# Kernel tuning notes

Measured on AMD Instinct MI355X. Metric: run time of the kernel, lower is better.

Reference implementation:

```python
import jax, jax.numpy as jnp
import numpy as np

TIME_STEPS = 100
SPIKE_THRESHOLD = 0.5
INPUT_DIM = 8192


def setup_inputs() -> dict:
    key = jax.random.key(0)
    k_x, k_w = jax.random.split(key)
    x = jax.random.uniform(k_x, (INPUT_DIM,), dtype=jnp.float32)
    # matches nn.Parameter(torch.rand(D, D) * 0.01)
    synaptic_weights = jax.random.uniform(k_w, (INPUT_DIM, INPUT_DIM), dtype=jnp.float32) * 0.01
    # matches nn.Parameter(torch.zeros(D))
    membrane_potential = jnp.zeros((INPUT_DIM,), dtype=jnp.float32)
    return {"x": x, "synaptic_weights": synaptic_weights, "membrane_potential": membrane_potential}


def reference(x, synaptic_weights, membrane_potential):
    # Drive is identical every timestep (x and W are loop-invariant), so compute once.
    drive = x @ synaptic_weights  # [D]

    def step(pot, _):
        pot = pot + drive
        spike = (pot >= SPIKE_THRESHOLD).astype(pot.dtype)  # spike_mask.float()
        pot = pot * (1.0 - spike)  # membrane_potential[spike_mask] = 0
        return pot, (spike, pot)

    _, (spikes, potentials) = jax.lax.scan(step, membrane_potential, None, length=TIME_STEPS)
    synaptic_activity = jnp.abs(synaptic_weights).mean()
    # spikes: [T, D], potentials: [T, D], synaptic_activity: scalar
    return spikes, potentials, synaptic_activity
```

## Files before the change

kernel.cpp:

```cpp
#include <hip/hip_runtime.h>

#define D 8192
#define T_STEPS 100
#define SPIKE_THR 0.5f
#define BLOCK 256
#define COLS_PER_THREAD 4
#define NCHUNK 256
#define ROWS_PER_CHUNK (D / NCHUNK)
#define COLBLOCKS (D / (BLOCK * COLS_PER_THREAD))

__global__ void __launch_bounds__(BLOCK)
k_partial(const float* __restrict__ x, const float* __restrict__ W,
          float* __restrict__ ws_drive, float* __restrict__ ws_abs) {
    __shared__ float xs[ROWS_PER_CHUNK];
    __shared__ float red[BLOCK];

    const int chunk = blockIdx.y;
    const int row0  = chunk * ROWS_PER_CHUNK;
    if (threadIdx.x < ROWS_PER_CHUNK)
        xs[threadIdx.x] = x[row0 + threadIdx.x];
    __syncthreads();

    const int j0 = (blockIdx.x * BLOCK + threadIdx.x) * COLS_PER_THREAD;

    float ax = 0.f, ay = 0.f, az = 0.f, aw = 0.f;
    float asum = 0.f;
    #pragma unroll
    for (int i = 0; i < ROWS_PER_CHUNK; ++i) {
        const float xv = xs[i];
        const float4 w = *reinterpret_cast<const float4*>(
            &W[(size_t)(row0 + i) * D + j0]);
        ax = fmaf(xv, w.x, ax);
        ay = fmaf(xv, w.y, ay);
        az = fmaf(xv, w.z, az);
        aw = fmaf(xv, w.w, aw);
        asum += fabsf(w.x) + fabsf(w.y) + fabsf(w.z) + fabsf(w.w);
    }

    float4 acc; acc.x = ax; acc.y = ay; acc.z = az; acc.w = aw;
    *reinterpret_cast<float4*>(&ws_drive[(size_t)chunk * D + j0]) = acc;

    red[threadIdx.x] = asum;
    __syncthreads();
    for (int s = BLOCK / 2; s > 0; s >>= 1) {
        if (threadIdx.x < s) red[threadIdx.x] += red[threadIdx.x + s];
        __syncthreads();
    }
    if (threadIdx.x == 0)
        ws_abs[blockIdx.y * gridDim.x + blockIdx.x] = red[0];
}

__global__ void __launch_bounds__(BLOCK)
k_sim(const float* __restrict__ ws_drive, const float* __restrict__ ws_abs,
      const float* __restrict__ pot0, float* __restrict__ out) {
    if (blockIdx.x == COLBLOCKS) {
        __shared__ float red[BLOCK];
        const int n = NCHUNK * COLBLOCKS;
        float s = 0.f;
        for (int i = threadIdx.x; i < n; i += BLOCK) s += ws_abs[i];
        red[threadIdx.x] = s;
        __syncthreads();
        for (int st = BLOCK / 2; st > 0; st >>= 1) {
            if (threadIdx.x < st) red[threadIdx.x] += red[threadIdx.x + st];
            __syncthreads();
        }
        if (threadIdx.x == 0)
            out[(size_t)2 * T_STEPS * D] = red[0] / ((float)D * (float)D);
        return;
    }

    const int j0 = (blockIdx.x * BLOCK + threadIdx.x) * COLS_PER_THREAD;

    float dx = 0.f, dy = 0.f, dz = 0.f, dw = 0.f;
    #pragma unroll 8
    for (int c = 0; c < NCHUNK; ++c) {
        const float4 p = *reinterpret_cast<const float4*>(
            &ws_drive[(size_t)c * D + j0]);
        dx += p.x; dy += p.y; dz += p.z; dw += p.w;
    }

    const float4 p0 = *reinterpret_cast<const float4*>(&pot0[j0]);
    float px = p0.x, py = p0.y, pz = p0.z, pw = p0.w;

    float* __restrict__ spikes = out;
    float* __restrict__ pots   = out + (size_t)T_STEPS * D;

    for (int t = 0; t < T_STEPS; ++t) {
        px += dx; py += dy; pz += dz; pw += dw;
        float4 sp;
        sp.x = (px >= SPIKE_THR) ? 1.f : 0.f;
        sp.y = (py >= SPIKE_THR) ? 1.f : 0.f;
        sp.z = (pz >= SPIKE_THR) ? 1.f : 0.f;
        sp.w = (pw >= SPIKE_THR) ? 1.f : 0.f;
        px *= (1.f - sp.x); py *= (1.f - sp.y);
        pz *= (1.f - sp.z); pw *= (1.f - sp.w);
        *reinterpret_cast<float4*>(&spikes[(size_t)t * D + j0]) = sp;
        float4 pv; pv.x = px; pv.y = py; pv.z = pz; pv.w = pw;
        *reinterpret_cast<float4*>(&pots[(size_t)t * D + j0]) = pv;
    }
}

extern "C" void kernel_launch(void* const* d_in, const int* in_sizes, int n_in,
                              void* d_out, int out_size, void* d_ws, size_t ws_size,
                              hipStream_t stream) {
    const float* x   = (const float*)d_in[0];
    const float* W   = (const float*)d_in[1];
    const float* mp0 = (const float*)d_in[2];
    float* out = (float*)d_out;

    float* ws_drive = (float*)d_ws;
    float* ws_abs   = ws_drive + (size_t)NCHUNK * D;

    dim3 g1(COLBLOCKS, NCHUNK);
    k_partial<<<g1, BLOCK, 0, stream>>>(x, W, ws_drive, ws_abs);
    k_sim<<<COLBLOCKS + 1, BLOCK, 0, stream>>>(ws_drive, ws_abs, mp0, out);
}
```

Before: 67.58 us.

## Split drive reduction into own kernel and parallelize simulation over time chunks

Moves the cross-chunk drive reduction into a separate k_reduce kernel (33 blocks) that writes one drive vector. The simulation kernel then runs on a 2D grid over column blocks and chunks of 4 timesteps. Each block replays the earlier timesteps in registers so it can write its own chunk without a serial dependency. The aim is to spread the 6.5 MB of spike and potential output writes across many more blocks than the previous 8, at the cost of an extra launch and redundant recomputation. The unroll count in k_partial also drops from full to 8.

After: 66.25 us. 2.0% less time.

```diff
diff --git a/kernel.cpp b/kernel.cpp
--- a/kernel.cpp
+++ b/kernel.cpp
@@ -8,6 +8,8 @@
 #define NCHUNK 256
 #define ROWS_PER_CHUNK (D / NCHUNK)
 #define COLBLOCKS (D / (BLOCK * COLS_PER_THREAD))
+#define STEPS_PER 4
+#define TCHUNKS (T_STEPS / STEPS_PER)
 
 __global__ void __launch_bounds__(BLOCK)
 k_partial(const float* __restrict__ x, const float* __restrict__ W,
@@ -25,7 +27,7 @@
 
     float ax = 0.f, ay = 0.f, az = 0.f, aw = 0.f;
     float asum = 0.f;
-    #pragma unroll
+    #pragma unroll 8
     for (int i = 0; i < ROWS_PER_CHUNK; ++i) {
         const float xv = xs[i];
         const float4 w = *reinterpret_cast<const float4*>(
@@ -51,9 +53,9 @@
 }
 
 __global__ void __launch_bounds__(BLOCK)
-k_sim(const float* __restrict__ ws_drive, const float* __restrict__ ws_abs,
-      const float* __restrict__ pot0, float* __restrict__ out) {
-    if (blockIdx.x == COLBLOCKS) {
+k_reduce(const float* __restrict__ ws_drive, const float* __restrict__ ws_abs,
+         float* __restrict__ drive, float* __restrict__ out) {
+    if (blockIdx.x == 32) {
         __shared__ float red[BLOCK];
         const int n = NCHUNK * COLBLOCKS;
         float s = 0.f;
@@ -68,25 +70,39 @@
             out[(size_t)2 * T_STEPS * D] = red[0] / ((float)D * (float)D);
         return;
     }
+    const int j = blockIdx.x * BLOCK + threadIdx.x;
+    float s = 0.f;
+    #pragma unroll 8
+    for (int c = 0; c < NCHUNK; ++c)
+        s += ws_drive[(size_t)c * D + j];
+    drive[j] = s;
+}
 
+__global__ void __launch_bounds__(BLOCK)
+k_sim(const float* __restrict__ drive, const float* __restrict__ pot0,
+      float* __restrict__ out) {
     const int j0 = (blockIdx.x * BLOCK + threadIdx.x) * COLS_PER_THREAD;
+    const int t0 = blockIdx.y * STEPS_PER;
 
-    float dx = 0.f, dy = 0.f, dz = 0.f, dw = 0.f;
-    #pragma unroll 8
-    for (int c = 0; c < NCHUNK; ++c) {
-        const float4 p = *reinterpret_cast<const float4*>(
-            &ws_drive[(size_t)c * D + j0]);
-        dx += p.x; dy += p.y; dz += p.z; dw += p.w;
-    }
-
+    const float4 d  = *reinterpret_cast<const float4*>(&drive[j0]);
     const float4 p0 = *reinterpret_cast<const float4*>(&pot0[j0]);
     float px = p0.x, py = p0.y, pz = p0.z, pw = p0.w;
+
+    for (int t = 0; t < t0; ++t) {
+        px += d.x; py += d.y; pz += d.z; pw += d.w;
+        px = (px >= SPIKE_THR) ? 0.f : px;
+        py = (py >= SPIKE_THR) ? 0.f : py;
+        pz = (pz >= SPIKE_THR) ? 0.f : pz;
+        pw = (pw >= SPIKE_THR) ? 0.f : pw;
+    }
 
     float* __restrict__ spikes = out;
     float* __restrict__ pots   = out + (size_t)T_STEPS * D;
 
-    for (int t = 0; t < T_STEPS; ++t) {
-        px += dx; py += dy; pz += dz; pw += dw;
+    #pragma unroll
+    for (int s = 0; s < STEPS_PER; ++s) {
+        const int t = t0 + s;
+        px += d.x; py += d.y; pz += d.z; pw += d.w;
         float4 sp;
         sp.x = (px >= SPIKE_THR) ? 1.f : 0.f;
         sp.y = (py >= SPIKE_THR) ? 1.f : 0.f;
@@ -110,8 +126,11 @@
 
     float* ws_drive = (float*)d_ws;
     float* ws_abs   = ws_drive + (size_t)NCHUNK * D;
+    float* drive    = ws_abs + NCHUNK * COLBLOCKS;
 
     dim3 g1(COLBLOCKS, NCHUNK);
     k_partial<<<g1, BLOCK, 0, stream>>>(x, W, ws_drive, ws_abs);
-    k_sim<<<COLBLOCKS + 1, BLOCK, 0, stream>>>(ws_drive, ws_abs, mp0, out);
+    k_reduce<<<33, BLOCK, 0, stream>>>(ws_drive, ws_abs, drive, out);
+    dim3 g3(COLBLOCKS, TCHUNKS);
+    k_sim<<<g3, BLOCK, 0, stream>>>(drive, mp0, out);
 }
```
